# Optimization experiments

Hardware: AMD Instinct MI355X
Metric: run time of the kernel (lower is better)

## Reference

```python
import jax, jax.numpy as jnp
import numpy as np

TAU = 1.0
F_BIAS = 1.0
EPS = 1e-5


def chunk_ln(x, g, b, n):
    # layernorm applied independently over n chunks of the last dim
    B, D = x.shape
    d = D // n
    xr = x.reshape(B, n, d)
    mu = xr.mean(axis=2, keepdims=True)
    var = xr.var(axis=2, keepdims=True)
    xr = (xr - mu) / jnp.sqrt(var + EPS)
    return xr.reshape(B, D) * g + b


def setup_inputs() -> dict:
    key = jax.random.key(0)
    ks = jax.random.split(key, 16)
    B, X, H, M, K = 256, 512, 1024, 128, 64
    inp = {
        "x": jax.random.normal(ks[0], (B, X), jnp.float32),
        "c": jax.random.normal(ks[1], (B, H), jnp.float32),
        "hmem": jax.random.normal(ks[2], (B, M, H), jnp.float32),
        "u_t": jax.random.uniform(ks[3], (B, M), jnp.float32),
        "prev_read_location": jnp.zeros((B, M), jnp.float32),
        "gumbel_u": jax.random.uniform(ks[4], (B, M), jnp.float32, minval=1e-6, maxval=1.0),
        "keys": jax.random.normal(ks[5], (M, K), jnp.float32) * 0.1,
        "vec_a": jax.random.normal(ks[6], (H // 4, 1), jnp.float32) * 0.1,
        "fc_w": jax.random.normal(ks[7], (X + 2 * H + K + M, H // 4), jnp.float32) * (1.0 / np.sqrt(X + 2 * H + K + M)),
        "fc_b": jnp.zeros((H // 4,), jnp.float32),
        "W_full": jax.random.normal(ks[8], (X + 2 * H, 5 * H), jnp.float32) * (1.0 / np.sqrt(X + 2 * H)),
        "bias": jnp.zeros((5 * H,), jnp.float32),
        "W_full1": jax.random.normal(ks[9], (X + 2 * H, 2 * H), jnp.float32) * (1.0 / np.sqrt(X + 2 * H)),
        "bias1": jnp.zeros((2 * H,), jnp.float32),
        "ln1_g": jnp.ones((5 * H,), jnp.float32), "ln1_b": jnp.zeros((5 * H,), jnp.float32),
        "ln2_g": jnp.ones((H,), jnp.float32), "ln2_b": jnp.zeros((H,), jnp.float32),
        "ln3_g": jnp.ones((2 * H,), jnp.float32), "ln3_b": jnp.zeros((2 * H,), jnp.float32),
        "ln4_g": jnp.ones((M,), jnp.float32), "ln4_b": jnp.zeros((M,), jnp.float32),
    }
    return inp


def reference(x, c, hmem, u_t, prev_read_location, gumbel_u,
              keys, vec_a, fc_w, fc_b, W_full, bias, W_full1, bias1,
              ln1_g, ln1_b, ln2_g, ln2_b, ln3_g, ln3_b, ln4_g, ln4_b):
    B, X = x.shape
    H = c.shape[1]
    M = keys.shape[0]
    # --- content-addressed read head ---
    xc = jnp.concatenate([x, c], axis=1)                      # [B, X+H]
    u_norm = u_t / jnp.maximum(jnp.linalg.norm(u_t, axis=1, keepdims=True), 1e-12)
    feat = jnp.concatenate([
        jnp.broadcast_to(xc[:, None, :], (B, M, xc.shape[1])),
        jnp.broadcast_to(keys[None, :, :], (B, M, keys.shape[1])),
        hmem,
        jnp.broadcast_to(u_norm[:, None, :], (B, M, M)),
    ], axis=2)                                                # [B, M, X+2H+K+M]
    hfeat = jnp.tanh(feat @ fc_w + fc_b)                      # [B, M, H//4]
    score = jnp.einsum('bmk,k->bm', hfeat, vec_a[:, 0])       # [B, M]
    score = score - prev_read_location * 100.0
    score = chunk_ln(score, ln4_g, ln4_b, 1)
    # --- gumbel-softmax hard read (straight-through) ---
    gumbel = -jnp.log(1e-20 - jnp.log(1e-20 + gumbel_u))
    y = jax.nn.softmax((score + gumbel) * TAU, axis=1)
    ymax = jnp.max(y, axis=1, keepdims=True)
    hard = (y == ymax).astype(y.dtype)
    h_read_index = jax.lax.stop_gradient(hard - y) + y        # one-hot fwd, soft bwd
    h_entry = jnp.einsum('bm,bmh->bh', h_read_index, hmem)    # [B, H]
    # --- gated LSTM-style cell ---
    concat0 = jnp.concatenate([x, c, h_entry], axis=1)        # [B, X+2H]
    g1 = jax.nn.sigmoid(chunk_ln(concat0 @ W_full1 + bias1, ln3_g, ln3_b, 2))
    gate = jnp.concatenate([jnp.ones_like(x), g1], axis=1)
    concat0 = concat0 * gate
    z = chunk_ln(concat0 @ W_full + bias, ln1_g, ln1_b, 5)
    i, j, f, o, om = jnp.split(z, 5, axis=1)
    new_c = c * jax.nn.sigmoid(f + F_BIAS) + jax.nn.sigmoid(i) * jnp.tanh(j)
    new_c = chunk_ln(new_c, ln2_g, ln2_b, 1)
    new_h = jnp.tanh(new_c) * jax.nn.sigmoid(o)
    r = jnp.tanh(h_entry) * jax.nn.sigmoid(om)
    new_r = jnp.concatenate([new_h, r], axis=1)               # [B, 2H]
    return new_r
```

## Files before the change

### kernel.cpp

```cpp
#include <hip/hip_runtime.h>
#include <cstdint>
#include <cstddef>

typedef unsigned short u16;
typedef float floatx4 __attribute__((ext_vector_type(4)));
typedef __bf16 bf16x8 __attribute__((ext_vector_type(8)));
typedef unsigned short u16x8 __attribute__((ext_vector_type(8)));
typedef unsigned short u16x4 __attribute__((ext_vector_type(4)));

__device__ __forceinline__ u16 f2bf(float f) {
  unsigned u = __float_as_uint(f);
  unsigned r = u + 0x7FFFu + ((u >> 16) & 1u);
  return (u16)(r >> 16);
}
__device__ __forceinline__ float bf2f(u16 h) {
  return __uint_as_float(((unsigned)h) << 16);
}
__device__ __forceinline__ void gl_lds16(const void* g, void* l) {
  __builtin_amdgcn_global_load_lds(
      (const __attribute__((address_space(1))) unsigned int*)g,
      (__attribute__((address_space(3))) unsigned int*)l, 16, 0, 0);
}
__device__ __forceinline__ float wsum(float v) {
#pragma unroll
  for (int m = 32; m > 0; m >>= 1) v += __shfl_xor(v, m, 64);
  return v;
}
__device__ __forceinline__ float wmaxr(float v) {
#pragma unroll
  for (int m = 32; m > 0; m >>= 1) v = fmaxf(v, __shfl_xor(v, m, 64));
  return v;
}
template <int NW>
__device__ __forceinline__ float bsum(float v, float* sh) {
  int lane = threadIdx.x & 63, wid = threadIdx.x >> 6;
  v = wsum(v);
  __syncthreads();
  if (lane == 0) sh[wid] = v;
  __syncthreads();
  float t = 0.f;
#pragma unroll
  for (int i = 0; i < NW; ++i) t += sh[i];
  return t;
}
template <int NW>
__device__ __forceinline__ float bmaxr(float v, float* sh) {
  int lane = threadIdx.x & 63, wid = threadIdx.x >> 6;
  v = wmaxr(v);
  __syncthreads();
  if (lane == 0) sh[wid] = v;
  __syncthreads();
  float t = sh[0];
#pragma unroll
  for (int i = 1; i < NW; ++i) t = fmaxf(t, sh[i]);
  return t;
}
__device__ __forceinline__ float sigm(float x) { return 1.0f / (1.0f + expf(-x)); }

__global__ __launch_bounds__(256) void k_prep(
    const float* __restrict__ fcw, const float* __restrict__ keys,
    const float* __restrict__ ut, const float* __restrict__ fcb,
    u16* __restrict__ W3H, u16* __restrict__ W3L,
    float* __restrict__ A2, float* __restrict__ UN) {
  __shared__ float kr[64];
  __shared__ float shs[4];
  int blk = blockIdx.x, t = threadIdx.x;
  if (blk < 128) {
    int ks = blk >> 2, q = blk & 3;
    int slot = q ^ ((t >> 1) & 3);
    u16x8 vh, vl;
#pragma unroll
    for (int e = 0; e < 8; ++e) {
      float f = fcw[(size_t)(1600 + ks * 32 + q * 8 + e) * 256 + t];
      u16 h = f2bf(f);
      vh[e] = h;
      vl[e] = f2bf(f - bf2f(h));
    }
    *(u16x8*)&W3H[(size_t)ks * 8192 + t * 32 + slot * 8] = vh;
    *(u16x8*)&W3L[(size_t)ks * 8192 + t * 32 + slot * 8] = vl;
  } else if (blk < 256) {
    int m = blk - 128;
    if (t < 64) kr[t] = keys[m * 64 + t];
    __syncthreads();
    float acc = fcb[t];
#pragma unroll 8
    for (int j = 0; j < 64; ++j)
      acc = fmaf(kr[j], fcw[(size_t)(1536 + j) * 256 + t], acc);
    A2[m * 256 + t] = acc;
  } else {
    int b = blk - 256;
    float v = (t < 128) ? ut[b * 128 + t] : 0.f;
    float s = bsum<4>(v * v, shs);
    float dnm = fmaxf(sqrtf(s), 1e-12f);
    if (t < 128) UN[b * 128 + t] = v / dnm;
  }
}

__global__ __launch_bounds__(256) void k_a1(
    const float* __restrict__ x, const float* __restrict__ c,
    const float* __restrict__ un, const float* __restrict__ fcw,
    float* __restrict__ A1) {
  __shared__ float sh[512];
  int kc = blockIdx.x % 26;
  int bg = blockIdx.x / 26;
  int t = threadIdx.x;
  int g0 = kc * 64;
  int row_base = (g0 < 1536) ? g0 : g0 + 1088;
#pragma unroll
  for (int p = 0; p < 2; ++p) {
    int idx = p * 256 + t;
    int bl = idx >> 6, j = idx & 63;
    int b = bg * 8 + bl;
    int g = g0 + j;
    float v;
    if (g < 512) v = x[b * 512 + g];
    else if (g < 1536) v = c[b * 1024 + (g - 512)];
    else v = un[b * 128 + (g - 1536)];
    sh[idx] = v;
  }
  __syncthreads();
  float acc[8];
#pragma unroll
  for (int i = 0; i < 8; ++i) acc[i] = 0.f;
#pragma unroll 4
  for (int j = 0; j < 64; ++j) {
    float wv = fcw[(size_t)(row_base + j) * 256 + t];
#pragma unroll
    for (int bl = 0; bl < 8; ++bl)
      acc[bl] = fmaf(sh[bl * 64 + j], wv, acc[bl]);
  }
#pragma unroll
  for (int bl = 0; bl < 8; ++bl)
    atomicAdd(&A1[(bg * 8 + bl) * 256 + t], acc[bl]);
}

__global__ __launch_bounds__(256, 2) void k2_score(
    const float* __restrict__ hmem, const u16* __restrict__ Bhp,
    const u16* __restrict__ Blp, const float* __restrict__ A1,
    const float* __restrict__ A2, const float* __restrict__ va,
    float* __restrict__ sp) {
  __shared__ __align__(16) u16 Ah[2][2048];
  __shared__ __align__(16) u16 Al[2][2048];
  __shared__ __align__(16) u16 Bh[2][8192];
  __shared__ __align__(16) u16 Bl[2][8192];
  const int b = blockIdx.x >> 1, hf = blockIdx.x & 1;
  const int t = threadIdx.x;
  const int lane = t & 63, w = t >> 6;
  const int q = lane >> 4, r16 = lane & 15;
  const int cq = w;
  const int slot = q ^ ((r16 >> 1) & 3);

  floatx4 acc[4][4];
#pragma unroll
  for (int i = 0; i < 4; ++i)
#pragma unroll
    for (int j = 0; j < 4; ++j) acc[i][j] = (floatx4){0.f, 0.f, 0.f, 0.f};

  const int m_st = t >> 2, qh = t & 3;
  const int wslot = qh ^ ((m_st >> 1) & 3);
  const int aw_idx = m_st * 32 + wslot * 8;
  const float* aptr = hmem + ((size_t)(b * 128 + hf * 64 + m_st)) * 1024 + qh * 8;

  int aoff[4], boff[4];
#pragma unroll
  for (int i = 0; i < 4; ++i) aoff[i] = (i * 16 + r16) * 32 + slot * 8;
#pragma unroll
  for (int ct = 0; ct < 4; ++ct) boff[ct] = (cq * 64 + ct * 16 + r16) * 32 + slot * 8;

#pragma unroll
  for (int i = 0; i < 4; ++i) {
    int L = (w * 4 + i) * 1024 + lane * 16;
    gl_lds16((const char*)Bhp + L, (char*)&Bh[0][0] + L);
    gl_lds16((const char*)Blp + L, (char*)&Bl[0][0] + L);
  }
  float pv[8];
#pragma unroll
  for (int i = 0; i < 8; ++i) pv[i] = aptr[i];
  {
    u16x8 hh, ll;
#pragma unroll
    for (int i = 0; i < 8; ++i) {
      u16 h = f2bf(pv[i]);
      hh[i] = h;
      ll[i] = f2bf(pv[i] - bf2f(h));
    }
    *(u16x8*)&Ah[0][aw_idx] = hh;
    *(u16x8*)&Al[0][aw_idx] = ll;
  }
#pragma unroll
  for (int i = 0; i < 8; ++i) pv[i] = aptr[32 + i];

  for (int ks = 0; ks < 32; ++ks) {
    const int cur = ks & 1, nxt = cur ^ 1;
    __syncthreads();
    if (ks < 31) {
#pragma unroll
      for (int i = 0; i < 4; ++i) {
        int L = (w * 4 + i) * 1024 + lane * 16;
        gl_lds16((const char*)Bhp + (size_t)(ks + 1) * 16384 + L, (char*)&Bh[nxt][0] + L);
        gl_lds16((const char*)Blp + (size_t)(ks + 1) * 16384 + L, (char*)&Bl[nxt][0] + L);
      }
      u16x8 hh, ll;
#pragma unroll
      for (int i = 0; i < 8; ++i) {
        u16 h = f2bf(pv[i]);
        hh[i] = h;
        ll[i] = f2bf(pv[i] - bf2f(h));
      }
      *(u16x8*)&Ah[nxt][aw_idx] = hh;
      *(u16x8*)&Al[nxt][aw_idx] = ll;
      if (ks < 30) {
        const float* np = aptr + (ks + 2) * 32;
#pragma unroll
        for (int i = 0; i < 8; ++i) pv[i] = np[i];
      }
    }
    bf16x8 ah[4], al[4];
#pragma unroll
    for (int i = 0; i < 4; ++i) {
      ah[i] = __builtin_bit_cast(bf16x8, *(const u16x8*)&Ah[cur][aoff[i]]);
      al[i] = __builtin_bit_cast(bf16x8, *(const u16x8*)&Al[cur][aoff[i]]);
    }
#pragma unroll
    for (int ct = 0; ct < 4; ++ct) {
      bf16x8 bh = __builtin_bit_cast(bf16x8, *(const u16x8*)&Bh[cur][boff[ct]]);
      bf16x8 bl = __builtin_bit_cast(bf16x8, *(const u16x8*)&Bl[cur][boff[ct]]);
#pragma unroll
      for (int i = 0; i < 4; ++i) {
        acc[i][ct] = __builtin_amdgcn_mfma_f32_16x16x32_bf16(ah[i], bh, acc[i][ct], 0, 0, 0);
        acc[i][ct] = __builtin_amdgcn_mfma_f32_16x16x32_bf16(ah[i], bl, acc[i][ct], 0, 0, 0);
        acc[i][ct] = __builtin_amdgcn_mfma_f32_16x16x32_bf16(al[i], bh, acc[i][ct], 0, 0, 0);
      }
    }
  }
  float rs[4][4];
#pragma unroll
  for (int i = 0; i < 4; ++i)
#pragma unroll
    for (int r = 0; r < 4; ++r) rs[i][r] = 0.f;
#pragma unroll
  for (int ct = 0; ct < 4; ++ct) {
    int col = cq * 64 + ct * 16 + r16;
    float a1v = A1[b * 256 + col];
    float vav = va[col];
#pragma unroll
    for (int i = 0; i < 4; ++i) {
      int m0 = hf * 64 + i * 16 + q * 4;
#pragma unroll
      for (int r = 0; r < 4; ++r) {
        float pre = acc[i][ct][r] + a1v + A2[(m0 + r) * 256 + col];
        rs[i][r] += tanhf(pre) * vav;
      }
    }
  }
#pragma unroll
  for (int mask = 1; mask <= 8; mask <<= 1)
#pragma unroll
    for (int i = 0; i < 4; ++i)
#pragma unroll
      for (int r = 0; r < 4; ++r) rs[i][r] += __shfl_xor(rs[i][r], mask, 64);
  if (r16 == 0) {
#pragma unroll
    for (int i = 0; i < 4; ++i)
#pragma unroll
      for (int r = 0; r < 4; ++r) {
        int row = hf * 64 + i * 16 + q * 4 + r;
        sp[cq * 32768 + b * 128 + row] = rs[i][r];
      }
  }
}

__global__ __launch_bounds__(256) void k34(
    const float* __restrict__ sp, const float* __restrict__ prev,
    const float* __restrict__ gu, const float* __restrict__ g4,
    const float* __restrict__ b4, const float* __restrict__ hmem,
    const float* __restrict__ x, const float* __restrict__ c,
    float* __restrict__ he, u16* __restrict__ ab1) {
  __shared__ float wsw[128];
  __shared__ float shs[4];
  int b = blockIdx.x, t = threadIdx.x;
  bool act = (t < 128);
  float s = 0.f;
  if (act) {
    int bm = b * 128 + t;
    s = sp[bm] + sp[32768 + bm] + sp[65536 + bm] + sp[98304 + bm] - prev[bm] * 100.0f;
  }
  float mu = bsum<4>(s, shs) * (1.0f / 128.0f);
  float d = act ? (s - mu) : 0.f;
  float var = bsum<4>(d * d, shs) * (1.0f / 128.0f);
  float z = -INFINITY;
  if (act) {
    float sn = d / sqrtf(var + 1e-5f) * g4[t] + b4[t];
    float gv = -logf(1e-20f - logf(1e-20f + gu[b * 128 + t]));
    z = sn + gv;
  }
  float zm = bmaxr<4>(z, shs);
  float e = act ? expf(z - zm) : 0.f;
  float Zs = bsum<4>(e, shs);
  float y = e / Zs;
  float ym = bmaxr<4>(y, shs);
  if (act) {
    float hard = (y == ym) ? 1.0f : 0.0f;
    wsw[t] = (hard - y) + y;
  }
  __syncthreads();
  float4 a;
  a.x = a.y = a.z = a.w = 0.f;
  for (int mm = 0; mm < 128; ++mm) {
    float wm = wsw[mm];
    if (wm != 0.0f) {
      float4 v = ((const float4*)(hmem + ((size_t)(b * 128 + mm)) * 1024))[t];
      a.x = fmaf(wm, v.x, a.x);
      a.y = fmaf(wm, v.y, a.y);
      a.z = fmaf(wm, v.z, a.z);
      a.w = fmaf(wm, v.w, a.w);
    }
  }
  ((float4*)(he + (size_t)b * 1024))[t] = a;
  const int sx = ((b >> 1) & 3) << 3;
  u16* row = ab1 + (size_t)b * 2560;
  if (t < 128) {
    float4 xv = ((const float4*)(x + (size_t)b * 512))[t];
    u16x4 o = {f2bf(xv.x), f2bf(xv.y), f2bf(xv.z), f2bf(xv.w)};
    *(u16x4*)&row[(t * 4) ^ sx] = o;
  }
  {
    float4 cv = ((const float4*)(c + (size_t)b * 1024))[t];
    u16x4 o = {f2bf(cv.x), f2bf(cv.y), f2bf(cv.z), f2bf(cv.w)};
    *(u16x4*)&row[(512 + t * 4) ^ sx] = o;
  }
  {
    u16x4 o = {f2bf(a.x), f2bf(a.y), f2bf(a.z), f2bf(a.w)};
    *(u16x4*)&row[(1536 + t * 4) ^ sx] = o;
  }
}

__global__ __launch_bounds__(256) void gemm_cell(
    const u16* __restrict__ Abf, const float* __restrict__ W,
    float* __restrict__ Zp, int N, int nblk, int nsteps) {
  __shared__ __align__(16) u16 Asm[256 * 32];
  __shared__ __align__(16) float Bf[32 * 64];
  __shared__ __align__(16) u16 Bsm[64 * 40];
  int cb = blockIdx.x % nblk;
  int kc = blockIdx.x / nblk;
  int t = threadIdx.x, lane = t & 63, w = t >> 6;
  int q = lane >> 4, r16 = lane & 15;
  const int axor = ((r16 >> 1) & 3) << 3;
  floatx4 acc[4][4];
#pragma unroll
  for (int i = 0; i < 4; ++i)
#pragma unroll
    for (int j = 0; j < 4; ++j) acc[i][j] = (floatx4){0.f, 0.f, 0.f, 0.f};
  int k0 = kc * nsteps * 32;
  for (int ks = 0; ks < nsteps; ++ks) {
    int k = k0 + ks * 32;
#pragma unroll
    for (int i = 0; i < 4; ++i) {
      int L = (w * 4 + i) * 1024 + lane * 16;
      int row = L >> 6, off = L & 63;
      gl_lds16((const char*)Abf + (size_t)row * 5120 + k * 2 + off, (char*)Asm + L);
    }
#pragma unroll
    for (int i = 0; i < 2; ++i) {
      int L = (w * 2 + i) * 1024 + lane * 16;
      int kr = L >> 8, off = L & 255;
      gl_lds16((const char*)W + ((size_t)(k + kr) * N + cb * 64) * 4 + off, (char*)Bf + L);
    }
    __syncthreads();
    {
      int cc = t & 63, p = t >> 6;
      u16x8 hh;
#pragma unroll
      for (int i2 = 0; i2 < 8; ++i2) hh[i2] = f2bf(Bf[(p * 8 + i2) * 64 + cc]);
      *(u16x8*)&Bsm[cc * 40 + p * 8] = hh;
    }
    __syncthreads();
    bf16x8 af[4];
#pragma unroll
    for (int i = 0; i < 4; ++i) {
      int row = w * 64 + i * 16 + r16;
      af[i] = __builtin_bit_cast(bf16x8, *(const u16x8*)&Asm[(row * 32 + q * 8) ^ axor]);
    }
#pragma unroll
    for (int ct = 0; ct < 4; ++ct) {
      int col = ct * 16 + r16;
      bf16x8 bb = __builtin_bit_cast(bf16x8, *(const u16x8*)&Bsm[col * 40 + q * 8]);
#pragma unroll
      for (int i = 0; i < 4; ++i)
        acc[i][ct] = __builtin_amdgcn_mfma_f32_16x16x32_bf16(af[i], bb, acc[i][ct], 0, 0, 0);
    }
    __syncthreads();
  }
  float* dst = Zp + (size_t)kc * 256 * N;
#pragma unroll
  for (int ct = 0; ct < 4; ++ct)
#pragma unroll
    for (int i = 0; i < 4; ++i)
#pragma unroll
      for (int r = 0; r < 4; ++r) {
        int col = cb * 64 + ct * 16 + r16;
        int row = w * 64 + i * 16 + q * 4 + r;
        dst[(size_t)row * N + col] = acc[i][ct][r];
      }
}

__global__ __launch_bounds__(256) void k5b(
    const float* __restrict__ Z1p, const float* __restrict__ bias1,
    const float* __restrict__ x, const float* __restrict__ c,
    const float* __restrict__ he, const float* __restrict__ g3,
    const float* __restrict__ b3, u16* __restrict__ ab2) {
  __shared__ float shs[4];
  int b = blockIdx.x, t = threadIdx.x;
  const float4* bp = (const float4*)bias1;
  float4 q0 = bp[t], q1 = bp[256 + t];
  float za[4] = {q0.x, q0.y, q0.z, q0.w};
  float zb[4] = {q1.x, q1.y, q1.z, q1.w};
#pragma unroll
  for (int kc = 0; kc < 8; ++kc) {
    const float4* zp = (const float4*)(Z1p + (size_t)kc * 524288 + (size_t)b * 2048);
    float4 v0 = zp[t], v1 = zp[256 + t];
    za[0] += v0.x; za[1] += v0.y; za[2] += v0.z; za[3] += v0.w;
    zb[0] += v1.x; zb[1] += v1.y; zb[2] += v1.z; zb[3] += v1.w;
  }
  float g1a[4], g1b[4];
  {
    float s = za[0] + za[1] + za[2] + za[3];
    float mu = bsum<4>(s, shs) * (1.0f / 1024.0f);
    float ss = 0.f;
#pragma unroll
    for (int i = 0; i < 4; ++i) { float d = za[i] - mu; ss += d * d; }
    float var = bsum<4>(ss, shs) * (1.0f / 1024.0f);
    float r = sqrtf(var + 1e-5f);
    float4 gv = ((const float4*)g3)[t];
    float4 bv = ((const float4*)b3)[t];
    g1a[0] = sigm((za[0] - mu) / r * gv.x + bv.x);
    g1a[1] = sigm((za[1] - mu) / r * gv.y + bv.y);
    g1a[2] = sigm((za[2] - mu) / r * gv.z + bv.z);
    g1a[3] = sigm((za[3] - mu) / r * gv.w + bv.w);
  }
  {
    float s = zb[0] + zb[1] + zb[2] + zb[3];
    float mu = bsum<4>(s, shs) * (1.0f / 1024.0f);
    float ss = 0.f;
#pragma unroll
    for (int i = 0; i < 4; ++i) { float d = zb[i] - mu; ss += d * d; }
    float var = bsum<4>(ss, shs) * (1.0f / 1024.0f);
    float r = sqrtf(var + 1e-5f);
    float4 gv = ((const float4*)g3)[256 + t];
    float4 bv = ((const float4*)b3)[256 + t];
    g1b[0] = sigm((zb[0] - mu) / r * gv.x + bv.x);
    g1b[1] = sigm((zb[1] - mu) / r * gv.y + bv.y);
    g1b[2] = sigm((zb[2] - mu) / r * gv.z + bv.z);
    g1b[3] = sigm((zb[3] - mu) / r * gv.w + bv.w);
  }
  const int sx = ((b >> 1) & 3) << 3;
  u16* row = ab2 + (size_t)b * 2560;
  if (t < 128) {
    float4 xv = ((const float4*)(x + (size_t)b * 512))[t];
    u16x4 o = {f2bf(xv.x), f2bf(xv.y), f2bf(xv.z), f2bf(xv.w)};
    *(u16x4*)&row[(t * 4) ^ sx] = o;
  }
  {
    float4 cv = ((const float4*)(c + (size_t)b * 1024))[t];
    u16x4 o = {f2bf(cv.x * g1a[0]), f2bf(cv.y * g1a[1]), f2bf(cv.z * g1a[2]), f2bf(cv.w * g1a[3])};
    *(u16x4*)&row[(512 + t * 4) ^ sx] = o;
  }
  {
    float4 hv = ((const float4*)(he + (size_t)b * 1024))[t];
    u16x4 o = {f2bf(hv.x * g1b[0]), f2bf(hv.y * g1b[1]), f2bf(hv.z * g1b[2]), f2bf(hv.w * g1b[3])};
    *(u16x4*)&row[(1536 + t * 4) ^ sx] = o;
  }
}

__global__ __launch_bounds__(256) void k5d(
    const float* __restrict__ Z2p, const float* __restrict__ bias,
    const float* __restrict__ c, const float* __restrict__ he,
    const float* __restrict__ g1, const float* __restrict__ b1,
    const float* __restrict__ g2, const float* __restrict__ b2,
    float* __restrict__ out) {
  __shared__ float shs[4];
  int b = blockIdx.x, t = threadIdx.x;
  const float4* bp = (const float4*)bias;
  float z[5][4];
#pragma unroll
  for (int ci = 0; ci < 5; ++ci) {
    float4 bb = bp[ci * 256 + t];
    z[ci][0] = bb.x; z[ci][1] = bb.y; z[ci][2] = bb.z; z[ci][3] = bb.w;
  }
#pragma unroll
  for (int kc = 0; kc < 4; ++kc) {
    const float4* zp = (const float4*)(Z2p + (size_t)kc * 1310720 + (size_t)b * 5120);
#pragma unroll
    for (int ci = 0; ci < 5; ++ci) {
      float4 v = zp[ci * 256 + t];
      z[ci][0] += v.x; z[ci][1] += v.y; z[ci][2] += v.z; z[ci][3] += v.w;
    }
  }
#pragma unroll
  for (int ci = 0; ci < 5; ++ci) {
    float s = z[ci][0] + z[ci][1] + z[ci][2] + z[ci][3];
    float mu = bsum<4>(s, shs) * (1.0f / 1024.0f);
    float ss = 0.f;
#pragma unroll
    for (int i = 0; i < 4; ++i) { float d = z[ci][i] - mu; ss += d * d; }
    float var = bsum<4>(ss, shs) * (1.0f / 1024.0f);
    float r = sqrtf(var + 1e-5f);
    float4 gv = ((const float4*)g1)[ci * 256 + t];
    float4 bv = ((const float4*)b1)[ci * 256 + t];
    z[ci][0] = (z[ci][0] - mu) / r * gv.x + bv.x;
    z[ci][1] = (z[ci][1] - mu) / r * gv.y + bv.y;
    z[ci][2] = (z[ci][2] - mu) / r * gv.z + bv.z;
    z[ci][3] = (z[ci][3] - mu) / r * gv.w + bv.w;
  }
  float4 cv = ((const float4*)(c + (size_t)b * 1024))[t];
  float cvv[4] = {cv.x, cv.y, cv.z, cv.w};
  float nc[4];
#pragma unroll
  for (int i = 0; i < 4; ++i)
    nc[i] = cvv[i] * sigm(z[2][i] + 1.0f) + sigm(z[0][i]) * tanhf(z[1][i]);
  float s = nc[0] + nc[1] + nc[2] + nc[3];
  float mu = bsum<4>(s, shs) * (1.0f / 1024.0f);
  float ss = 0.f;
#pragma unroll
  for (int i = 0; i < 4; ++i) { float d = nc[i] - mu; ss += d * d; }
  float var = bsum<4>(ss, shs) * (1.0f / 1024.0f);
  float r2 = sqrtf(var + 1e-5f);
  float4 g2v = ((const float4*)g2)[t];
  float4 b2v = ((const float4*)b2)[t];
  float g2a[4] = {g2v.x, g2v.y, g2v.z, g2v.w};
  float b2a[4] = {b2v.x, b2v.y, b2v.z, b2v.w};
  float4 hv = ((const float4*)(he + (size_t)b * 1024))[t];
  float hva[4] = {hv.x, hv.y, hv.z, hv.w};
  float4 o1, o2;
  float nh[4], rr[4];
#pragma unroll
  for (int i = 0; i < 4; ++i) {
    float ncn = (nc[i] - mu) / r2 * g2a[i] + b2a[i];
    nh[i] = tanhf(ncn) * sigm(z[3][i]);
    rr[i] = tanhf(hva[i]) * sigm(z[4][i]);
  }
  o1.x = nh[0]; o1.y = nh[1]; o1.z = nh[2]; o1.w = nh[3];
  o2.x = rr[0]; o2.y = rr[1]; o2.z = rr[2]; o2.w = rr[3];
  ((float4*)(out + (size_t)b * 2048))[t] = o1;
  ((float4*)(out + (size_t)b * 2048 + 1024))[t] = o2;
}

extern "C" void kernel_launch(void* const* d_in, const int* in_sizes, int n_in,
                              void* d_out, int out_size, void* d_ws, size_t ws_size,
                              hipStream_t stream) {
  const float* x = (const float*)d_in[0];
  const float* c = (const float*)d_in[1];
  const float* hmem = (const float*)d_in[2];
  const float* ut = (const float*)d_in[3];
  const float* prev = (const float*)d_in[4];
  const float* gu = (const float*)d_in[5];
  const float* keys = (const float*)d_in[6];
  const float* veca = (const float*)d_in[7];
  const float* fcw = (const float*)d_in[8];
  const float* fcb = (const float*)d_in[9];
  const float* Wf = (const float*)d_in[10];
  const float* bias = (const float*)d_in[11];
  const float* Wf1 = (const float*)d_in[12];
  const float* bias1 = (const float*)d_in[13];
  const float* ln1g = (const float*)d_in[14];
  const float* ln1b = (const float*)d_in[15];
  const float* ln2g = (const float*)d_in[16];
  const float* ln2b = (const float*)d_in[17];
  const float* ln3g = (const float*)d_in[18];
  const float* ln3b = (const float*)d_in[19];
  const float* ln4g = (const float*)d_in[20];
  const float* ln4b = (const float*)d_in[21];

  char* ws = (char*)d_ws;
  float* UN = (float*)(ws + 0);
  float* A2 = (float*)(ws + 131072);
  float* A1 = (float*)(ws + 262144);
  u16* W3H = (u16*)(ws + 524288);
  u16* W3L = (u16*)(ws + 1048576);
  float* SP = (float*)(ws + 1572864);
  float* HE = (float*)(ws + 2097152);
  u16* AB1 = (u16*)(ws + 3145728);
  u16* AB2 = (u16*)(ws + 4456448);
  float* Z1p = (float*)(ws + 5767168);
  float* Z2p = (float*)(ws + 22544384);

  hipMemsetAsync(A1, 0, (size_t)256 * 256 * 4, stream);
  k_prep<<<512, 256, 0, stream>>>(fcw, keys, ut, fcb, W3H, W3L, A2, UN);
  k_a1<<<832, 256, 0, stream>>>(x, c, UN, fcw, A1);
  k2_score<<<512, 256, 0, stream>>>(hmem, W3H, W3L, A1, A2, veca, SP);
  k34<<<256, 256, 0, stream>>>(SP, prev, gu, ln4g, ln4b, hmem, x, c, HE, AB1);
  gemm_cell<<<32 * 8, 256, 0, stream>>>(AB1, Wf1, Z1p, 2048, 32, 10);
  k5b<<<256, 256, 0, stream>>>(Z1p, bias1, x, c, HE, ln3g, ln3b, AB2);
  gemm_cell<<<80 * 4, 256, 0, stream>>>(AB2, Wf, Z2p, 5120, 80, 20);
  k5d<<<256, 256, 0, stream>>>(Z2p, bias, c, HE, ln1g, ln1b, ln2g, ln2b, (float*)d_out);
}
```

Baseline: 426.5 us.

## Split score and cell GEMM column tiles to double block count

The score kernel now splits the 256 output columns across two blocks per (batch, half). Each wave loads its B fragments (pre-laid-out by k_prep in MFMA fragment order) straight from global into registers, so the B tiles no longer pass through LDS. This frees LDS so four blocks can share a CU, and the partial-sum buffer grows from 4 to 8 parts, which k34 now reduces. The cell GEMMs switch to 32-column tiles, doubling the grid for more parallelism. The trade-off is more redundant A-side conversion and hmem reads per block, plus more partial-sum traffic.

```diff
diff --git a/kernel.cpp b/kernel.cpp
--- a/kernel.cpp
+++ b/kernel.cpp
@@ -66,18 +66,20 @@
   __shared__ float shs[4];
   int blk = blockIdx.x, t = threadIdx.x;
   if (blk < 128) {
-    int ks = blk >> 2, q = blk & 3;
-    int slot = q ^ ((t >> 1) & 3);
+    int ks = blk >> 2, qq = blk & 3;
+    int tc = qq * 4 + (t >> 6);
+    int lane = t & 63, q = lane >> 4, r16 = lane & 15;
     u16x8 vh, vl;
 #pragma unroll
-    for (int e = 0; e < 8; ++e) {
-      float f = fcw[(size_t)(1600 + ks * 32 + q * 8 + e) * 256 + t];
+    for (int j = 0; j < 8; ++j) {
+      float f = fcw[(size_t)(1600 + ks * 32 + q * 8 + j) * 256 + tc * 16 + r16];
       u16 h = f2bf(f);
-      vh[e] = h;
-      vl[e] = f2bf(f - bf2f(h));
-    }
-    *(u16x8*)&W3H[(size_t)ks * 8192 + t * 32 + slot * 8] = vh;
-    *(u16x8*)&W3L[(size_t)ks * 8192 + t * 32 + slot * 8] = vl;
+      vh[j] = h;
+      vl[j] = f2bf(f - bf2f(h));
+    }
+    size_t o = (((size_t)ks * 16 + tc) * 64 + lane) * 8;
+    *(u16x8*)&W3H[o] = vh;
+    *(u16x8*)&W3L[o] = vl;
   } else if (blk < 256) {
     int m = blk - 128;
     if (t < 64) kr[t] = keys[m * 64 + t];
@@ -134,45 +136,45 @@
     atomicAdd(&A1[(bg * 8 + bl) * 256 + t], acc[bl]);
 }
 
-__global__ __launch_bounds__(256, 2) void k2_score(
-    const float* __restrict__ hmem, const u16* __restrict__ Bhp,
-    const u16* __restrict__ Blp, const float* __restrict__ A1,
+__global__ __launch_bounds__(256, 4) void k2_score(
+    const float* __restrict__ hmem, const u16* __restrict__ W3H,
+    const u16* __restrict__ W3L, const float* __restrict__ A1,
     const float* __restrict__ A2, const float* __restrict__ va,
     float* __restrict__ sp) {
   __shared__ __align__(16) u16 Ah[2][2048];
   __shared__ __align__(16) u16 Al[2][2048];
-  __shared__ __align__(16) u16 Bh[2][8192];
-  __shared__ __align__(16) u16 Bl[2][8192];
-  const int b = blockIdx.x >> 1, hf = blockIdx.x & 1;
+  const int bi = blockIdx.x;
+  const int b = bi >> 2, hf = (bi >> 1) & 1, ch = bi & 1;
   const int t = threadIdx.x;
   const int lane = t & 63, w = t >> 6;
   const int q = lane >> 4, r16 = lane & 15;
-  const int cq = w;
   const int slot = q ^ ((r16 >> 1) & 3);
 
-  floatx4 acc[4][4];
+  floatx4 acc[4][2];
 #pragma unroll
   for (int i = 0; i < 4; ++i)
 #pragma unroll
-    for (int j = 0; j < 4; ++j) acc[i][j] = (floatx4){0.f, 0.f, 0.f, 0.f};
+    for (int j = 0; j < 2; ++j) acc[i][j] = (floatx4){0.f, 0.f, 0.f, 0.f};
 
   const int m_st = t >> 2, qh = t & 3;
   const int wslot = qh ^ ((m_st >> 1) & 3);
   const int aw_idx = m_st * 32 + wslot * 8;
   const float* aptr = hmem + ((size_t)(b * 128 + hf * 64 + m_st)) * 1024 + qh * 8;
 
-  int aoff[4], boff[4];
+  int aoff[4];
 #pragma unroll
   for (int i = 0; i < 4; ++i) aoff[i] = (i * 16 + r16) * 32 + slot * 8;
-#pragma unroll
-  for (int ct = 0; ct < 4; ++ct) boff[ct] = (cq * 64 + ct * 16 + r16) * 32 + slot * 8;
-
-#pragma unroll
-  for (int i = 0; i < 4; ++i) {
-    int L = (w * 4 + i) * 1024 + lane * 16;
-    gl_lds16((const char*)Bhp + L, (char*)&Bh[0][0] + L);
-    gl_lds16((const char*)Blp + L, (char*)&Bl[0][0] + L);
-  }
+
+  const int tc0 = ch * 8 + w * 2;
+  const u16* pBH = W3H + ((size_t)tc0 * 64 + lane) * 8;
+  const u16* pBL = W3L + ((size_t)tc0 * 64 + lane) * 8;
+
+  u16x8 bhC[2], blC[2], bhN[2], blN[2];
+  bhC[0] = *(const u16x8*)(pBH);
+  bhC[1] = *(const u16x8*)(pBH + 512);
+  blC[0] = *(const u16x8*)(pBL);
+  blC[1] = *(const u16x8*)(pBL + 512);
+
   float pv[8];
 #pragma unroll
   for (int i = 0; i < 8; ++i) pv[i] = aptr[i];
@@ -190,57 +192,73 @@
 #pragma unroll
   for (int i = 0; i < 8; ++i) pv[i] = aptr[32 + i];
 
+  auto stageA = [&](int buf) {
+    u16x8 hh, ll;
+#pragma unroll
+    for (int i = 0; i < 8; ++i) {
+      u16 h = f2bf(pv[i]);
+      hh[i] = h;
+      ll[i] = f2bf(pv[i] - bf2f(h));
+    }
+    *(u16x8*)&Ah[buf][aw_idx] = hh;
+    *(u16x8*)&Al[buf][aw_idx] = ll;
+  };
+  auto comp = [&](int buf, u16x8* bh, u16x8* bl) {
+    bf16x8 ah[4], al[4];
+#pragma unroll
+    for (int i = 0; i < 4; ++i) {
+      ah[i] = __builtin_bit_cast(bf16x8, *(const u16x8*)&Ah[buf][aoff[i]]);
+      al[i] = __builtin_bit_cast(bf16x8, *(const u16x8*)&Al[buf][aoff[i]]);
+    }
+#pragma unroll
+    for (int ct = 0; ct < 2; ++ct) {
+      bf16x8 bhv = __builtin_bit_cast(bf16x8, bh[ct]);
+      bf16x8 blv = __builtin_bit_cast(bf16x8, bl[ct]);
+#pragma unroll
+      for (int i = 0; i < 4; ++i) {
+        acc[i][ct] = __builtin_amdgcn_mfma_f32_16x16x32_bf16(ah[i], bhv, acc[i][ct], 0, 0, 0);
+        acc[i][ct] = __builtin_amdgcn_mfma_f32_16x16x32_bf16(ah[i], blv, acc[i][ct], 0, 0, 0);
+        acc[i][ct] = __builtin_amdgcn_mfma_f32_16x16x32_bf16(al[i], bhv, acc[i][ct], 0, 0, 0);
+      }
+    }
+  };
+
+#pragma unroll 2
   for (int ks = 0; ks < 32; ++ks) {
-    const int cur = ks & 1, nxt = cur ^ 1;
     __syncthreads();
+    const int cur = ks & 1;
     if (ks < 31) {
-#pragma unroll
-      for (int i = 0; i < 4; ++i) {
-        int L = (w * 4 + i) * 1024 + lane * 16;
-        gl_lds16((const char*)Bhp + (size_t)(ks + 1) * 16384 + L, (char*)&Bh[nxt][0] + L);
-        gl_lds16((const char*)Blp + (size_t)(ks + 1) * 16384 + L, (char*)&Bl[nxt][0] + L);
+      const size_t so = (size_t)(ks + 1) * 8192;
+      if (cur == 0) {
+        bhN[0] = *(const u16x8*)(pBH + so);
+        bhN[1] = *(const u16x8*)(pBH + so + 512);
+        blN[0] = *(const u16x8*)(pBL + so);
+        blN[1] = *(const u16x8*)(pBL + so + 512);
+      } else {
+        bhC[0] = *(const u16x8*)(pBH + so);
+        bhC[1] = *(const u16x8*)(pBH + so + 512);
+        blC[0] = *(const u16x8*)(pBL + so);
+        blC[1] = *(const u16x8*)(pBL + so + 512);
       }
-      u16x8 hh, ll;
-#pragma unroll
-      for (int i = 0; i < 8; ++i) {
-        u16 h = f2bf(pv[i]);
-        hh[i] = h;
-        ll[i] = f2bf(pv[i] - bf2f(h));
-      }
-      *(u16x8*)&Ah[nxt][aw_idx] = hh;
-      *(u16x8*)&Al[nxt][aw_idx] = ll;
+      stageA(cur ^ 1);
       if (ks < 30) {
         const float* np = aptr + (ks + 2) * 32;
 #pragma unroll
         for (int i = 0; i < 8; ++i) pv[i] = np[i];
       }
     }
-    bf16x8 ah[4], al[4];
-#pragma unroll
-    for (int i = 0; i < 4; ++i) {
-      ah[i] = __builtin_bit_cast(bf16x8, *(const u16x8*)&Ah[cur][aoff[i]]);
-      al[i] = __builtin_bit_cast(bf16x8, *(const u16x8*)&Al[cur][aoff[i]]);
-    }
-#pragma unroll
-    for (int ct = 0; ct < 4; ++ct) {
-      bf16x8 bh = __builtin_bit_cast(bf16x8, *(const u16x8*)&Bh[cur][boff[ct]]);
-      bf16x8 bl = __builtin_bit_cast(bf16x8, *(const u16x8*)&Bl[cur][boff[ct]]);
-#pragma unroll
-      for (int i = 0; i < 4; ++i) {
-        acc[i][ct] = __builtin_amdgcn_mfma_f32_16x16x32_bf16(ah[i], bh, acc[i][ct], 0, 0, 0);
-        acc[i][ct] = __builtin_amdgcn_mfma_f32_16x16x32_bf16(ah[i], bl, acc[i][ct], 0, 0, 0);
-        acc[i][ct] = __builtin_amdgcn_mfma_f32_16x16x32_bf16(al[i], bh, acc[i][ct], 0, 0, 0);
-      }
-    }
-  }
+    if (cur == 0) comp(0, bhC, blC);
+    else comp(1, bhN, blN);
+  }
+
   float rs[4][4];
 #pragma unroll
   for (int i = 0; i < 4; ++i)
 #pragma unroll
     for (int r = 0; r < 4; ++r) rs[i][r] = 0.f;
 #pragma unroll
-  for (int ct = 0; ct < 4; ++ct) {
-    int col = cq * 64 + ct * 16 + r16;
+  for (int ct = 0; ct < 2; ++ct) {
+    int col = ch * 128 + w * 32 + ct * 16 + r16;
     float a1v = A1[b * 256 + col];
     float vav = va[col];
 #pragma unroll
@@ -260,12 +278,13 @@
 #pragma unroll
       for (int r = 0; r < 4; ++r) rs[i][r] += __shfl_xor(rs[i][r], mask, 64);
   if (r16 == 0) {
+    int part = ch * 4 + w;
 #pragma unroll
     for (int i = 0; i < 4; ++i)
 #pragma unroll
       for (int r = 0; r < 4; ++r) {
         int row = hf * 64 + i * 16 + q * 4 + r;
-        sp[cq * 32768 + b * 128 + row] = rs[i][r];
+        sp[part * 32768 + b * 128 + row] = rs[i][r];
       }
   }
 }
@@ -283,7 +302,9 @@
   float s = 0.f;
   if (act) {
     int bm = b * 128 + t;
-    s = sp[bm] + sp[32768 + bm] + sp[65536 + bm] + sp[98304 + bm] - prev[bm] * 100.0f;
+#pragma unroll
+    for (int p = 0; p < 8; ++p) s += sp[p * 32768 + bm];
+    s -= prev[bm] * 100.0f;
   }
   float mu = bsum<4>(s, shs) * (1.0f / 128.0f);
   float d = act ? (s - mu) : 0.f;
@@ -339,18 +360,18 @@
     const u16* __restrict__ Abf, const float* __restrict__ W,
     float* __restrict__ Zp, int N, int nblk, int nsteps) {
   __shared__ __align__(16) u16 Asm[256 * 32];
-  __shared__ __align__(16) float Bf[32 * 64];
-  __shared__ __align__(16) u16 Bsm[64 * 40];
+  __shared__ __align__(16) float Bf[32 * 32];
+  __shared__ __align__(16) u16 Bsm[32 * 40];
   int cb = blockIdx.x % nblk;
   int kc = blockIdx.x / nblk;
   int t = threadIdx.x, lane = t & 63, w = t >> 6;
   int q = lane >> 4, r16 = lane & 15;
   const int axor = ((r16 >> 1) & 3) << 3;
-  floatx4 acc[4][4];
+  floatx4 acc[4][2];
 #pragma unroll
   for (int i = 0; i < 4; ++i)
 #pragma unroll
-    for (int j = 0; j < 4; ++j) acc[i][j] = (floatx4){0.f, 0.f, 0.f, 0.f};
+    for (int j = 0; j < 2; ++j) acc[i][j] = (floatx4){0.f, 0.f, 0.f, 0.f};
   int k0 = kc * nsteps * 32;
   for (int ks = 0; ks < nsteps; ++ks) {
     int k = k0 + ks * 32;
@@ -360,19 +381,18 @@
       int row = L >> 6, off = L & 63;
       gl_lds16((const char*)Abf + (size_t)row * 5120 + k * 2 + off, (char*)Asm + L);
     }
-#pragma unroll
-    for (int i = 0; i < 2; ++i) {
-      int L = (w * 2 + i) * 1024 + lane * 16;
-      int kr = L >> 8, off = L & 255;
-      gl_lds16((const char*)W + ((size_t)(k + kr) * N + cb * 64) * 4 + off, (char*)Bf + L);
+    {
+      int L = t * 16;
+      int kr = L >> 7, off = L & 127;
+      gl_lds16((const char*)W + ((size_t)(k + kr) * N + cb * 32) * 4 + off, (char*)Bf + L);
     }
     __syncthreads();
     {
-      int cc = t & 63, p = t >> 6;
-      u16x8 hh;
-#pragma unroll
-      for (int i2 = 0; i2 < 8; ++i2) hh[i2] = f2bf(Bf[(p * 8 + i2) * 64 + cc]);
-      *(u16x8*)&Bsm[cc * 40 + p * 8] = hh;
+      int cc = t & 31, p = t >> 5;
+      u16x4 hh;
+#pragma unroll
+      for (int i2 = 0; i2 < 4; ++i2) hh[i2] = f2bf(Bf[(p * 4 + i2) * 32 + cc]);
+      *(u16x4*)&Bsm[cc * 40 + p * 4] = hh;
     }
     __syncthreads();
     bf16x8 af[4];
@@ -382,7 +402,7 @@
       af[i] = __builtin_bit_cast(bf16x8, *(const u16x8*)&Asm[(row * 32 + q * 8) ^ axor]);
     }
 #pragma unroll
-    for (int ct = 0; ct < 4; ++ct) {
+    for (int ct = 0; ct < 2; ++ct) {
       int col = ct * 16 + r16;
       bf16x8 bb = __builtin_bit_cast(bf16x8, *(const u16x8*)&Bsm[col * 40 + q * 8]);
 #pragma unroll
@@ -393,12 +413,12 @@
   }
   float* dst = Zp + (size_t)kc * 256 * N;
 #pragma unroll
-  for (int ct = 0; ct < 4; ++ct)
+  for (int ct = 0; ct < 2; ++ct)
 #pragma unroll
     for (int i = 0; i < 4; ++i)
 #pragma unroll
       for (int r = 0; r < 4; ++r) {
-        int col = cb * 64 + ct * 16 + r16;
+        int col = cb * 32 + ct * 16 + r16;
         int row = w * 64 + i * 16 + q * 4 + r;
         dst[(size_t)row * N + col] = acc[i][ct][r];
       }
@@ -578,19 +598,19 @@
   u16* W3H = (u16*)(ws + 524288);
   u16* W3L = (u16*)(ws + 1048576);
   float* SP = (float*)(ws + 1572864);
-  float* HE = (float*)(ws + 2097152);
-  u16* AB1 = (u16*)(ws + 3145728);
-  u16* AB2 = (u16*)(ws + 4456448);
-  float* Z1p = (float*)(ws + 5767168);
-  float* Z2p = (float*)(ws + 22544384);
+  float* HE = (float*)(ws + 2621440);
+  u16* AB1 = (u16*)(ws + 3670016);
+  u16* AB2 = (u16*)(ws + 4980736);
+  float* Z1p = (float*)(ws + 6291456);
+  float* Z2p = (float*)(ws + 23068672);
 
   hipMemsetAsync(A1, 0, (size_t)256 * 256 * 4, stream);
   k_prep<<<512, 256, 0, stream>>>(fcw, keys, ut, fcb, W3H, W3L, A2, UN);
   k_a1<<<832, 256, 0, stream>>>(x, c, UN, fcw, A1);
-  k2_score<<<512, 256, 0, stream>>>(hmem, W3H, W3L, A1, A2, veca, SP);
+  k2_score<<<1024, 256, 0, stream>>>(hmem, W3H, W3L, A1, A2, veca, SP);
   k34<<<256, 256, 0, stream>>>(SP, prev, gu, ln4g, ln4b, hmem, x, c, HE, AB1);
-  gemm_cell<<<32 * 8, 256, 0, stream>>>(AB1, Wf1, Z1p, 2048, 32, 10);
+  gemm_cell<<<64 * 8, 256, 0, stream>>>(AB1, Wf1, Z1p, 2048, 64, 10);
   k5b<<<256, 256, 0, stream>>>(Z1p, bias1, x, c, HE, ln3g, ln3b, AB2);
-  gemm_cell<<<80 * 4, 256, 0, stream>>>(AB2, Wf, Z2p, 5120, 80, 20);
+  gemm_cell<<<160 * 4, 256, 0, stream>>>(AB2, Wf, Z2p, 5120, 160, 20);
   k5d<<<256, 256, 0, stream>>>(Z2p, bias, c, HE, ln1g, ln1b, ln2g, ln2b, (float*)d_out);
 }
```

Result: faster. 408.7 us (-4.2%).
